# Kernel optimization log

Measured on AMD Instinct MI355X. Metric: run time of the kernel, lower is better.

## Reference

```python
import jax, jax.numpy as jnp
import numpy as np

N_NODES = 16384
K_NBR = 16
N_HOPS = 4  # hops + 2
IN_DIM = 256
RAW_DIM = 128
OUT_DIM = 64
PHI_DIM = 16
N_KERN = 4
E = N_NODES * K_NBR


def setup_inputs() -> dict:
    key = jax.random.key(0)
    ks = jax.random.split(key, 16)
    s = 0.05  # small weight scale for numerical sanity
    h = jax.random.normal(ks[0], (N_NODES, IN_DIM), jnp.float32)
    e_tensor = jax.random.normal(ks[1], (N_HOPS, N_NODES, RAW_DIM), jnp.float32)
    # kNN-style edges: each dst node has exactly K_NBR incoming edges
    src = jax.random.randint(ks[2], (N_HOPS, E), 0, N_NODES, jnp.int32)
    dst = jnp.tile(jnp.repeat(jnp.arange(N_NODES, dtype=jnp.int32), K_NBR)[None, :], (N_HOPS, 1))
    return {
        'h': h,
        'e_tensor': e_tensor,
        'src': src,
        'dst': dst,
        'W_phi': jax.random.normal(ks[3], (N_HOPS, RAW_DIM, PHI_DIM - 1), jnp.float32) * s,
        'mlp_w1': jax.random.normal(ks[4], (N_HOPS, RAW_DIM, IN_DIM), jnp.float32) * s,
        'mlp_b1': jax.random.normal(ks[5], (N_HOPS, IN_DIM), jnp.float32) * s,
        'mlp_w2': jax.random.normal(ks[6], (N_HOPS, IN_DIM, PHI_DIM * N_KERN), jnp.float32) * s,
        'mlp_b2': jax.random.normal(ks[7], (N_HOPS, PHI_DIM * N_KERN), jnp.float32) * s,
        'tilde_phi': jax.random.normal(ks[8], (N_HOPS, N_KERN, PHI_DIM), jnp.float32),
        'W': jax.random.normal(ks[9], (N_HOPS, IN_DIM, OUT_DIM * N_KERN), jnp.float32) * s,
        'bias': jax.random.normal(ks[10], (N_HOPS, OUT_DIM), jnp.float32) * s,
        'z': jax.random.normal(ks[11], (OUT_DIM, 1), jnp.float32),
    }


def _deform_gconv(h, e_l, src, dst, W_phi, w1, b1, w2, b2, tilde_phi, W, bias):
    N = h.shape[0]
    nk, phi_dim = tilde_phi.shape
    hk = (h @ W).reshape(N, nk, -1)                                  # (N, nk, out)
    phi = e_l @ W_phi                                                # (N, phi-1)
    tn = tilde_phi / jnp.linalg.norm(tilde_phi, axis=1, keepdims=True)  # (nk, phi)
    hid = jax.nn.relu(e_l @ w1 + b1)
    delta = (hid @ w2 + b2).reshape(N, nk, phi_dim)                  # (N, nk, phi)
    delta_ik = tn[None, :, :] + delta                                # (N, nk, phi)
    # per-edge quantities (edges carry dst-node delta_ik, u_sub_v distance)
    dist = phi[src] - phi[dst]                                       # (E, phi-1)
    last = jnp.all(dist == 0, axis=1, keepdims=True).astype(dist.dtype)
    dist = jnp.concatenate([dist, last], axis=1)                     # (E, phi)
    dist = dist / jnp.maximum(jnp.linalg.norm(dist, axis=1, keepdims=True), 1e-8)
    logits = jnp.einsum('ep,ekp->ek', dist, delta_ik[dst])           # (E, nk)
    # edge_softmax over incoming edges of each dst node
    mx = jax.ops.segment_max(logits, dst, num_segments=N)
    ex = jnp.exp(logits - mx[dst])
    den = jax.ops.segment_sum(ex, dst, num_segments=N)
    att = ex / den[dst]                                              # (E, nk)
    # message passing: m = h[src] * att, sum over incoming edges
    m = hk[src] * att[:, :, None]                                    # (E, nk, out)
    agg = jax.ops.segment_sum(m, dst, num_segments=N)                # (N, nk, out)
    out = agg.sum(1) + bias[None, :]
    out = out / jnp.maximum(jnp.linalg.norm(out, axis=1, keepdims=True), 1e-8)
    # regularizers
    d = tn[:, None, :] - tn[None, :, :]                              # (nk, nk, phi)
    l_sep = jnp.sum(jnp.sum(d * d, axis=-1)) / nk                    # sum_i mean_j ||t_i - t_j||^2
    l_focus = jnp.mean(jnp.sum(delta * delta, axis=2))
    return out, l_sep, l_focus


def reference(h, e_tensor, src, dst, W_phi, mlp_w1, mlp_b1, mlp_w2, mlp_b2, tilde_phi, W, bias, z):
    outs, l_seps, l_fos = jax.vmap(
        _deform_gconv, in_axes=(None, 0, 0, 0, 0, 0, 0, 0, 0, 0, 0, 0)
    )(h, e_tensor, src, dst, W_phi, mlp_w1, mlp_b1, mlp_w2, mlp_b2, tilde_phi, W, bias)
    # hop-level softmax fusion
    score = jnp.einsum('hno,oz->hnz', outs, z)                       # (n_hops, N, 1)
    att = jax.nn.softmax(score, axis=0)
    tilde_h = jnp.sum(att * outs, axis=0)                            # (N, out)
    l_sep = jnp.mean(l_seps)
    l_focus = jnp.mean(l_fos)
    return tilde_h, l_sep, l_focus
```

## Files before the change

kernel.cpp:

```cpp
#include <hip/hip_runtime.h>
#include <hip/hip_bf16.h>

#define N_NODES 16384
#define K_NBR 16
#define HOPS 4
#define IN_DIM 256
#define RAW_DIM 128
#define OUT_DIM 64
#define PHI_DIM 16
#define N_KERN 4
#define E_EDGES (N_NODES * K_NBR)

typedef __hip_bfloat16 bf16;
typedef __attribute__((ext_vector_type(8))) short short8;
typedef __attribute__((ext_vector_type(4))) float f32x4;
typedef __attribute__((ext_vector_type(4))) unsigned int uint4v;

__device__ __forceinline__ float toF(float x) { return x; }
__device__ __forceinline__ float toF(bf16 x) { return __bfloat162float(x); }
__device__ __forceinline__ short f2bfbits(float f)
{
    bf16 b = __float2bfloat16(f);
    short s; __builtin_memcpy(&s, &b, 2); return s;
}

#define SWZ(row, colShort) ((colShort) ^ (((row) & 7) << 3))

__device__ __forceinline__ void gld_lds16(const bf16* g, short* l)
{
    __builtin_amdgcn_global_load_lds(
        (const __attribute__((address_space(1))) unsigned int*)g,
        (__attribute__((address_space(3))) unsigned int*)l, 16, 0, 0);
}

#define CV_WPHI 0
#define CV_W1   (CV_WPHI + HOPS * RAW_DIM * (PHI_DIM - 1))
#define CV_B1   (CV_W1 + HOPS * RAW_DIM * IN_DIM)
#define CV_W2   (CV_B1 + HOPS * IN_DIM)
#define CV_B2   (CV_W2 + HOPS * IN_DIM * PHI_DIM * N_KERN)
#define CV_TPHI (CV_B2 + HOPS * PHI_DIM * N_KERN)
#define CV_W    (CV_TPHI + HOPS * N_KERN * PHI_DIM)
#define CV_BIAS (CV_W + HOPS * IN_DIM * OUT_DIM * N_KERN)
#define CV_Z    (CV_BIAS + HOPS * OUT_DIM)
#define CV_END  (CV_Z + OUT_DIM)

#define WT_N  (HOPS * 256 * 256)
#define W1T_N (HOPS * 256 * 128)
#define W2T_N (HOPS * 64 * 256)
#define WPT_N (HOPS * 16 * 128)
#define CVT_TOTAL (WT_N + W1T_N + W2T_N + WPT_N)

#define NB_CV ((CV_END + 255) / 256)
#define NB_WT (CVT_TOTAL / 256)
#define NB_H  (N_NODES * 256 / 8 / 256)
#define NB_E  (HOPS * N_NODES * 128 / 8 / 256)
#define NB_ALL (NB_CV + NB_WT + NB_H + NB_E + 1)

#define GA_NA 1536
#define GA_NB 1024
#define GA_TOTAL (GA_NA + GA_NB)

__device__ __forceinline__ float loadDyn(const void* p, int i, bool isbf)
{
    return isbf ? toF(((const bf16*)p)[i]) : ((const float*)p)[i];
}

__device__ __forceinline__ void cvt8(bf16* dst, const void* src, size_t base, bool isbf)
{
    short8 v;
    if (isbf) {
        v = *(const short8*)((const bf16*)src + base);
    } else {
        const float* sp = (const float*)src + base;
        f32x4 f0 = *(const f32x4*)sp;
        f32x4 f1 = *(const f32x4*)(sp + 4);
#pragma unroll
        for (int j = 0; j < 4; j++) { v[j] = f2bfbits(f0[j]); v[4 + j] = f2bfbits(f1[j]); }
    }
    *(short8*)(dst + base) = v;
}

__global__ __launch_bounds__(256) void cvt_all(
    const void* h, const void* e,
    const void* wphi, const void* w1, const void* b1, const void* w2,
    const void* b2, const void* tphi, const void* W, const void* bias,
    const void* z, float* __restrict__ CV,
    bf16* __restrict__ wt, bf16* __restrict__ w1t, bf16* __restrict__ w2t,
    bf16* __restrict__ wpt, bf16* __restrict__ h_bf, bf16* __restrict__ e_bf,
    float* __restrict__ tn_out, float* __restrict__ acc, int* __restrict__ flagOut)
{
    __shared__ float s_det[4];
    int tid = threadIdx.x;
    {
        unsigned short pv = ((const unsigned short*)h)[tid];
        unsigned int bits = ((unsigned int)pv) << 16;
        float v; __builtin_memcpy(&v, &bits, 4);
        v = fabsf(v);
        if (!(v == v) || v > 1e30f) v = 1e30f;
#pragma unroll
        for (int off = 32; off > 0; off >>= 1) v = fmaxf(v, __shfl_xor(v, off));
        if ((tid & 63) == 0) s_det[tid >> 6] = v;
    }
    __syncthreads();
    bool isbf = fmaxf(fmaxf(s_det[0], s_det[1]), fmaxf(s_det[2], s_det[3])) < 1e4f;

    int b = blockIdx.x;
    if (b == NB_ALL - 1) {
        __shared__ float s_v[256], s_tn[256], s_red[256], s_hop[4];
        int hop = tid >> 6, t64 = tid & 63;
        int row = t64 >> 4, p = t64 & 15;
        float v = loadDyn(tphi, hop * 64 + t64, isbf);
        s_v[tid] = v;
        __syncthreads();
        float ss = 0.f;
        for (int q = 0; q < 16; q++) { float x = s_v[hop * 64 + row * 16 + q]; ss += x * x; }
        float tnv = v / sqrtf(ss);
        tn_out[hop * 64 + t64] = tnv;
        s_tn[tid] = tnv;
        __syncthreads();
        float s = 0.f;
        for (int j = 0; j < 4; j++) {
            float d = tnv - s_tn[hop * 64 + j * 16 + p];
            s += d * d;
        }
        s_red[tid] = s;
        __syncthreads();
        if (t64 == 0) {
            float tot = 0.f;
            for (int i = 0; i < 64; i++) tot += s_red[hop * 64 + i];
            s_hop[hop] = tot;
        }
        __syncthreads();
        if (tid == 0) {
            acc[0] = (s_hop[0] + s_hop[1] + s_hop[2] + s_hop[3]) * 0.0625f;
            acc[1] = 0.f;
            *flagOut = isbf ? 1 : 0;
        }
        return;
    }
    if (b < NB_CV) {
        int idx = b * 256 + tid;
        if (idx >= CV_END) return;
        float v;
        if      (idx < CV_W1)   v = loadDyn(wphi, idx - CV_WPHI, isbf);
        else if (idx < CV_B1)   v = loadDyn(w1,   idx - CV_W1,   isbf);
        else if (idx < CV_W2)   v = loadDyn(b1,   idx - CV_B1,   isbf);
        else if (idx < CV_B2)   v = loadDyn(w2,   idx - CV_W2,   isbf);
        else if (idx < CV_TPHI) v = loadDyn(b2,   idx - CV_B2,   isbf);
        else if (idx < CV_W)    v = loadDyn(tphi, idx - CV_TPHI, isbf);
        else if (idx < CV_BIAS) v = loadDyn(W,    idx - CV_W,    isbf);
        else if (idx < CV_Z)    v = loadDyn(bias, idx - CV_BIAS, isbf);
        else                    v = loadDyn(z,    idx - CV_Z,    isbf);
        CV[idx] = v;
        return;
    }
    b -= NB_CV;
    if (b < NB_WT) {
        int idx = b * 256 + tid;
        if (idx < WT_N) {
            int o = idx, hop = o >> 16, rem = o & 65535, n = rem >> 8, k = rem & 255;
            wt[o] = __float2bfloat16(loadDyn(W, hop * 65536 + k * 256 + n, isbf));
        } else if (idx < WT_N + W1T_N) {
            int o = idx - WT_N, hop = o >> 15, rem = o & 32767, n = rem >> 7, k = rem & 127;
            w1t[o] = __float2bfloat16(loadDyn(w1, hop * 32768 + k * 256 + n, isbf));
        } else if (idx < WT_N + W1T_N + W2T_N) {
            int o = idx - WT_N - W1T_N, hop = o >> 14, rem = o & 16383, n = rem >> 8, k = rem & 255;
            w2t[o] = __float2bfloat16(loadDyn(w2, hop * 16384 + k * 64 + n, isbf));
        } else {
            int o = idx - WT_N - W1T_N - W2T_N, hop = o >> 11, rem = o & 2047, n = rem >> 7, k = rem & 127;
            float v = (n < 15) ? loadDyn(wphi, hop * 1920 + k * 15 + n, isbf) : 0.f;
            wpt[o] = __float2bfloat16(v);
        }
        return;
    }
    b -= NB_WT;
    if (b < NB_H) {
        size_t base = ((size_t)b * 256 + tid) * 8;
        cvt8(h_bf, h, base, isbf);
        return;
    }
    b -= NB_H;
    {
        size_t base = ((size_t)b * 256 + tid) * 8;
        cvt8(e_bf, e, base, isbf);
    }
}

template <int BN, int WR, int WC, int OUTMODE, bool STAGED>
__device__ __forceinline__ void gemm_dev(
    char* smem, const bf16* __restrict__ A, const bf16* __restrict__ Bt,
    void* __restrict__ Cg, int K, int N, int colBase, int rowBase)
{
    constexpr int WM = 128 / WR;
    constexpr int WN = BN / WC;
    constexpr int MT = WM / 16;
    constexpr int NT = WN / 16;
    constexpr int ESZ = (OUTMODE == 0) ? 4 : 1;
    short* As = (short*)smem;
    short* Bs = As + 128 * 64;

    int tid = threadIdx.x;
    int w = tid >> 6, lane = tid & 63;
    int wr = w / WC, wc = w % WC;
    int l16 = lane & 15, quad = lane >> 4;

    f32x4 acc[MT][NT] = {};

    for (int k0 = 0; k0 < K; k0 += 64) {
        for (int id = tid; id < 128 * 8; id += 256) {
            int row = id >> 3, j = id & 7;
            gld_lds16(A + (size_t)(rowBase + row) * K + k0 + ((j ^ (row & 7)) * 8),
                      As + id * 8);
        }
        for (int id = tid; id < BN * 8; id += 256) {
            int row = id >> 3, j = id & 7;
            gld_lds16(Bt + (size_t)(colBase + row) * K + k0 + ((j ^ (row & 7)) * 8),
                      Bs + id * 8);
        }
        __syncthreads();
#pragma unroll
        for (int kc = 0; kc < 64; kc += 32) {
            short8 aF[MT], bF[NT];
#pragma unroll
            for (int mi = 0; mi < MT; mi++) {
                int row = wr * WM + mi * 16 + l16;
                aF[mi] = *(const short8*)&As[row * 64 + SWZ(row, kc + quad * 8)];
            }
#pragma unroll
            for (int ni = 0; ni < NT; ni++) {
                int row = wc * WN + ni * 16 + l16;
                bF[ni] = *(const short8*)&Bs[row * 64 + SWZ(row, kc + quad * 8)];
            }
#pragma unroll
            for (int mi = 0; mi < MT; mi++)
#pragma unroll
                for (int ni = 0; ni < NT; ni++)
                    acc[mi][ni] = __builtin_amdgcn_mfma_f32_16x16x32_bf16(
                        aF[mi], bF[ni], acc[mi][ni], 0, 0, 0);
        }
        __syncthreads();
    }

#pragma unroll
    for (int mi = 0; mi < MT; mi++) {
#pragma unroll
        for (int ni = 0; ni < NT; ni++) {
            int cl = wc * WN + ni * 16 + l16;
            int col = colBase + cl;
#pragma unroll
            for (int r = 0; r < 4; r++) {
                int rl = wr * WM + mi * 16 + quad * 4 + r;
                float v = acc[mi][ni][r];
                if (STAGED) {
                    size_t idx = (size_t)rl * BN + cl;
                    if (OUTMODE == 0) ((float*)smem)[idx] = v;
                    else {
                        int pk = __builtin_amdgcn_cvt_pk_fp8_f32(v, v, 0, false);
                        ((unsigned char*)smem)[idx] = (unsigned char)(pk & 0xFF);
                    }
                } else {
                    ((float*)Cg)[(size_t)(rowBase + rl) * N + col] = v;
                }
            }
        }
    }
    if (STAGED) {
        __syncthreads();
        constexpr int CPR = BN * ESZ / 16;
        for (int c = tid; c < 128 * CPR; c += 256) {
            int r = c / CPR, off = (c % CPR) * 16;
            *(uint4v*)((char*)Cg + ((size_t)(rowBase + r) * N + colBase) * ESZ + off) =
                *(const uint4v*)(smem + (size_t)r * BN * ESZ + off);
        }
    }
}

__device__ __forceinline__ void hid_delta_dev(
    char* smem,
    const bf16* __restrict__ A, const bf16* __restrict__ B1,
    const bf16* __restrict__ B2, const float* __restrict__ b1,
    const float* __restrict__ b2, const float* __restrict__ tn,
    float* __restrict__ Dg, float* __restrict__ lfocus, int rowBase)
{
    short* As  = (short*)smem;
    short* Bs  = As + 64 * 64;
    short* Hs  = (short*)smem;
    short* B2s = Hs + 64 * 256;
    float* Ds  = (float*)smem;
    float* s_w = (float*)(smem + 64 * 256 * 2 + 64 * 64 * 2 - 16);

    int tid = threadIdx.x;
    int w = tid >> 6, lane = tid & 63;
    int l16 = lane & 15, quad = lane >> 4;

    {
        f32x4 acc[4][4] = {};
        for (int k0 = 0; k0 < 128; k0 += 64) {
            for (int id = tid; id < 64 * 8; id += 256) {
                int row = id >> 3, j = id & 7;
                gld_lds16(A + (size_t)(rowBase + row) * 128 + k0 + ((j ^ (row & 7)) * 8),
                          As + id * 8);
            }
            for (int id = tid; id < 256 * 8; id += 256) {
                int row = id >> 3, j = id & 7;
                gld_lds16(B1 + (size_t)row * 128 + k0 + ((j ^ (row & 7)) * 8),
                          Bs + id * 8);
            }
            __syncthreads();
#pragma unroll
            for (int kc = 0; kc < 64; kc += 32) {
                short8 aF[4], bF[4];
#pragma unroll
                for (int mi = 0; mi < 4; mi++) {
                    int row = mi * 16 + l16;
                    aF[mi] = *(const short8*)&As[row * 64 + SWZ(row, kc + quad * 8)];
                }
#pragma unroll
                for (int ni = 0; ni < 4; ni++) {
                    int row = w * 64 + ni * 16 + l16;
                    bF[ni] = *(const short8*)&Bs[row * 64 + SWZ(row, kc + quad * 8)];
                }
#pragma unroll
                for (int mi = 0; mi < 4; mi++)
#pragma unroll
                    for (int ni = 0; ni < 4; ni++)
                        acc[mi][ni] = __builtin_amdgcn_mfma_f32_16x16x32_bf16(
                            aF[mi], bF[ni], acc[mi][ni], 0, 0, 0);
            }
            __syncthreads();
        }
#pragma unroll
        for (int mi = 0; mi < 4; mi++) {
#pragma unroll
            for (int ni = 0; ni < 4; ni++) {
                int col = w * 64 + ni * 16 + l16;
                float bv = b1[col];
#pragma unroll
                for (int r = 0; r < 4; r++) {
                    int row = mi * 16 + quad * 4 + r;
                    float v = fmaxf(acc[mi][ni][r] + bv, 0.f);
                    Hs[row * 256 + SWZ(row, col)] = f2bfbits(v);
                }
            }
        }
        for (int id = tid; id < 64 * 8; id += 256) {
            int row = id >> 3, j = id & 7;
            gld_lds16(B2 + (size_t)row * 256 + ((j ^ (row & 7)) * 8),
                      B2s + id * 8);
        }
    }

    {
        f32x4 acc2[4] = {};
        for (int q = 0; q < 4; q++) {
            __syncthreads();
#pragma unroll
            for (int kcq = 0; kcq < 64; kcq += 32) {
                int arow = w * 16 + l16;
                short8 aF = *(const short8*)&Hs[arow * 256 + SWZ(arow, q * 64 + kcq + quad * 8)];
                short8 bF[4];
#pragma unroll
                for (int ni = 0; ni < 4; ni++) {
                    int row = ni * 16 + l16;
                    bF[ni] = *(const short8*)&B2s[row * 64 + SWZ(row, kcq + quad * 8)];
                }
#pragma unroll
                for (int ni = 0; ni < 4; ni++)
                    acc2[ni] = __builtin_amdgcn_mfma_f32_16x16x32_bf16(aF, bF[ni], acc2[ni], 0, 0, 0);
            }
            if (q < 3) {
                __syncthreads();
                for (int id = tid; id < 64 * 8; id += 256) {
                    int row = id >> 3, j = id & 7;
                    gld_lds16(B2 + (size_t)row * 256 + (q + 1) * 64 + ((j ^ (row & 7)) * 8),
                              B2s + id * 8);
                }
            }
        }
        __syncthreads();
        float sq = 0.f;
#pragma unroll
        for (int ni = 0; ni < 4; ni++) {
            int col = ni * 16 + l16;
            float bv = b2[col], tv = tn[col];
#pragma unroll
            for (int r = 0; r < 4; r++) {
                int row = w * 16 + quad * 4 + r;
                float v = acc2[ni][r] + bv;
                sq += v * v;
                Ds[row * 64 + col] = v + tv;
            }
        }
#pragma unroll
        for (int off = 32; off > 0; off >>= 1) sq += __shfl_xor(sq, off);
        if (lane == 0) s_w[w] = sq;
        __syncthreads();
        for (int c = tid; c < 64 * 16; c += 256) {
            int r = c >> 4, off = (c & 15) * 4;
            *(uint4v*)(Dg + (size_t)(rowBase + r) * 64 + off) =
                *(const uint4v*)(Ds + (size_t)r * 64 + off);
        }
        if (tid == 0) atomicAdd(lfocus, s_w[0] + s_w[1] + s_w[2] + s_w[3]);
    }
}

__global__ __launch_bounds__(256) void gemm_all(
    const bf16* __restrict__ h_bf, const bf16* __restrict__ e_bf,
    const bf16* __restrict__ WT, const bf16* __restrict__ WPT,
    const bf16* __restrict__ W1T, const bf16* __restrict__ W2T,
    const float* __restrict__ b1All, const float* __restrict__ b2All,
    const float* __restrict__ tnAll, unsigned char* __restrict__ hk_f8,
    float* __restrict__ phi, float* __restrict__ DELTA, float* __restrict__ lfocus)
{
    __shared__ __align__(16) char smem[64 * 256 * 2 + 64 * 64 * 2];
    int b = blockIdx.x;
    bool isA;
    int a;
    if (b < 2 * GA_NB) { isA = !(b & 1); a = b >> 1; }
    else               { isA = true;     a = GA_NB + (b - 2 * GA_NB); }
    if (isA) {
        int hop = a / 384, r = a % 384, part = r >> 7, row = r & 127;
        if (part < 2) {
            gemm_dev<128, 2, 2, 2, true>(
                smem, h_bf, WT + (size_t)hop * 256 * 256,
                hk_f8 + (size_t)hop * N_NODES * 256, 256, 256, part * 128, row * 128);
        } else {
            gemm_dev<16, 4, 1, 0, false>(
                smem, e_bf + (size_t)hop * N_NODES * 128, WPT + (size_t)hop * 16 * 128,
                phi + (size_t)hop * N_NODES * 16, 128, 16, 0, row * 128);
        }
    } else {
        int hop = a >> 8, tile = a & 255;
        hid_delta_dev(smem,
            e_bf + (size_t)hop * N_NODES * 128,
            W1T + (size_t)hop * 256 * 128, W2T + (size_t)hop * 64 * 256,
            b1All + hop * 256, b2All + hop * 64, tnAll + hop * 64,
            DELTA + (size_t)hop * N_NODES * 64, lfocus, tile * 64);
    }
}

__global__ __launch_bounds__(256) void edge_agg2(
    const unsigned char* __restrict__ hk, const float* __restrict__ phi,
    const float* __restrict__ dik, const int* __restrict__ src,
    const float* __restrict__ biasAll, float* __restrict__ outs)
{
    int b = blockIdx.x;
    int hop = b & 3;
    int wave = threadIdx.x >> 6, lane = threadIdx.x & 63;
    int node = (b >> 2) * 4 + wave;
    const unsigned char* hk_l = hk + (size_t)hop * N_NODES * 256;
    const float* phi_l  = phi + (size_t)hop * N_NODES * 16;
    const float* dik_l  = dik + (size_t)hop * N_NODES * 64;
    const int*   src_n  = src + (size_t)hop * E_EDGES + (size_t)node * 16;
    const float* bias_l = biasAll + hop * 64;
    float*       outs_n = outs + ((size_t)hop * N_NODES + node) * 64;

    __shared__ float s_dik[4][64];
    __shared__ __align__(16) float s_attT[4][4][24];
    __shared__ int   s_src[4][16];

    s_dik[wave][lane] = dik_l[(size_t)node * 64 + lane];
    if (lane < 16) s_src[wave][lane] = src_n[lane];

    int e = lane >> 2, q = lane & 3;
    int sN = s_src[wave][e];
    f32x4 ps = *(const f32x4*)(phi_l + (size_t)sN * 16 + q * 4);
    f32x4 pd = *(const f32x4*)(phi_l + (size_t)node * 16 + q * 4);
    float d0 = ps[0] - pd[0], d1 = ps[1] - pd[1];
    float d2 = ps[2] - pd[2], d3 = ps[3] - pd[3];
    bool q3 = (q == 3);
    float ssp = d0 * d0 + d1 * d1 + d2 * d2 + (q3 ? 0.f : d3 * d3);
    ssp += __shfl_xor(ssp, 1); ssp += __shfl_xor(ssp, 2);
    float last = (ssp == 0.f) ? 1.f : 0.f;
    if (q3) d3 = last;
    float inv = 1.f / fmaxf(sqrtf(ssp + last * last), 1e-8f);
#pragma unroll
    for (int k = 0; k < 4; k++) {
        const float* dk = &s_dik[wave][k * 16 + q * 4];
        float pk = d0 * dk[0] + d1 * dk[1] + d2 * dk[2] + d3 * dk[3];
        pk += __shfl_xor(pk, 1); pk += __shfl_xor(pk, 2);
        if (q == k) s_attT[wave][k][e] = pk * inv;
    }

    int k2 = lane & 3;
    float lgv = s_attT[wave][k2][e];
    float mx = lgv;
    mx = fmaxf(mx, __shfl_xor(mx, 4));
    mx = fmaxf(mx, __shfl_xor(mx, 8));
    mx = fmaxf(mx, __shfl_xor(mx, 16));
    mx = fmaxf(mx, __shfl_xor(mx, 32));
    float ex = __expf(lgv - mx);
    float den = ex;
    den += __shfl_xor(den, 4);
    den += __shfl_xor(den, 8);
    den += __shfl_xor(den, 16);
    den += __shfl_xor(den, 32);
    s_attT[wave][k2][e] = ex / den;

    int kk = lane >> 4, dsub = (lane & 15) * 4;
    f32x4 attv[4];
#pragma unroll
    for (int g = 0; g < 4; g++) attv[g] = *(const f32x4*)&s_attT[wave][kk][g * 4];
    float a0 = 0.f, a1 = 0.f, a2 = 0.f, a3 = 0.f;
#pragma unroll
    for (int ee = 0; ee < 16; ee++) {
        int sm = __builtin_amdgcn_readfirstlane(s_src[wave][ee]);
        unsigned int u = *(const unsigned int*)(hk_l + (size_t)sm * 256 + lane * 4);
        float wgt = attv[ee >> 2][ee & 3];
        auto lo = __builtin_amdgcn_cvt_pk_f32_fp8((int)u, false);
        auto hi = __builtin_amdgcn_cvt_pk_f32_fp8((int)u, true);
        a0 += wgt * lo[0];
        a1 += wgt * lo[1];
        a2 += wgt * hi[0];
        a3 += wgt * hi[1];
    }
    a0 += __shfl_xor(a0, 16); a0 += __shfl_xor(a0, 32);
    a1 += __shfl_xor(a1, 16); a1 += __shfl_xor(a1, 32);
    a2 += __shfl_xor(a2, 16); a2 += __shfl_xor(a2, 32);
    a3 += __shfl_xor(a3, 16); a3 += __shfl_xor(a3, 32);
    f32x4 bv = *(const f32x4*)(bias_l + dsub);
    float o0 = a0 + bv[0];
    float o1 = a1 + bv[1];
    float o2 = a2 + bv[2];
    float o3 = a3 + bv[3];
    float ssq = o0 * o0 + o1 * o1 + o2 * o2 + o3 * o3;
    ssq += __shfl_xor(ssq, 1);
    ssq += __shfl_xor(ssq, 2);
    ssq += __shfl_xor(ssq, 4);
    ssq += __shfl_xor(ssq, 8);
    float inv2 = 1.f / fmaxf(sqrtf(ssq), 1e-8f);
    if (kk == 0) {
        f32x4 st;
        st[0] = o0 * inv2; st[1] = o1 * inv2; st[2] = o2 * inv2; st[3] = o3 * inv2;
        *(f32x4*)(outs_n + dsub) = st;
    }
}

__global__ __launch_bounds__(256) void fuse_kernel(
    const float* __restrict__ outs, const float* __restrict__ z,
    void* __restrict__ out, const int* __restrict__ flag,
    const float* __restrict__ acc)
{
    int tid = threadIdx.x;
    int node = blockIdx.x * 4 + (tid >> 6);
    int dd = tid & 63;
    float zv = z[dd];
    float o[4], sc[4];
#pragma unroll
    for (int h = 0; h < 4; h++) {
        o[h] = outs[((size_t)h * N_NODES + node) * 64 + dd];
        float v = o[h] * zv;
#pragma unroll
        for (int off = 32; off > 0; off >>= 1) v += __shfl_xor(v, off);
        sc[h] = v;
    }
    float mx = fmaxf(fmaxf(sc[0], sc[1]), fmaxf(sc[2], sc[3]));
    float e0 = __expf(sc[0] - mx), e1 = __expf(sc[1] - mx);
    float e2 = __expf(sc[2] - mx), e3 = __expf(sc[3] - mx);
    float den = e0 + e1 + e2 + e3;
    float t = (e0 * o[0] + e1 * o[1] + e2 * o[2] + e3 * o[3]) / den;
    size_t oi = (size_t)node * 64 + dd;
    bool isbf = (*flag != 0);
    if (isbf) ((bf16*)out)[oi] = __float2bfloat16(t);
    else      ((float*)out)[oi] = t;
    if (blockIdx.x == 0 && tid == 0) {
        float a = acc[0];
        float b = acc[1] / ((float)N_NODES * 4.f * 4.f);
        size_t base = (size_t)N_NODES * 64;
        if (isbf) {
            ((bf16*)out)[base]     = __float2bfloat16(a);
            ((bf16*)out)[base + 1] = __float2bfloat16(b);
        } else {
            ((float*)out)[base]     = a;
            ((float*)out)[base + 1] = b;
        }
    }
}

extern "C" void kernel_launch(void* const* d_in, const int* in_sizes, int n_in,
                              void* d_out, int out_size, void* d_ws, size_t ws_size,
                              hipStream_t stream)
{
    const void* h    = d_in[0];
    const void* e    = d_in[1];
    const int*  src  = (const int*)d_in[2];
    const void* Wphi = d_in[4];
    const void* w1   = d_in[5];
    const void* b1   = d_in[6];
    const void* w2   = d_in[7];
    const void* b2   = d_in[8];
    const void* tphi = d_in[9];
    const void* W    = d_in[10];
    const void* bias = d_in[11];
    const void* z    = d_in[12];

    float* ws    = (float*)d_ws;
    float* CV    = ws;
    float* OUTS  = CV + CV_END;
    float* PHI   = OUTS + (size_t)4 * N_NODES * 64;
    float* DELTA = PHI + (size_t)4 * N_NODES * 16;
    float* TN    = DELTA + (size_t)4 * N_NODES * 64;
    float* ACC   = TN + 256;
    int*   FLAG  = (int*)(ACC + 2);
    bf16*  H_BF  = (bf16*)(ACC + 4);
    bf16*  E_BF  = H_BF + (size_t)N_NODES * 256;
    bf16*  WT    = E_BF + (size_t)HOPS * N_NODES * 128;
    bf16*  W1T   = WT + WT_N;
    bf16*  W2T   = W1T + W1T_N;
    bf16*  WPT   = W2T + W2T_N;
    unsigned char* HK_F8 = (unsigned char*)(WPT + WPT_N);

    cvt_all<<<NB_ALL, 256, 0, stream>>>(
        h, e, Wphi, w1, b1, w2, b2, tphi, W, bias, z, CV,
        WT, W1T, W2T, WPT, H_BF, E_BF, TN, ACC, FLAG);

    gemm_all<<<dim3(GA_TOTAL), 256, 0, stream>>>(
        H_BF, E_BF, WT, WPT, W1T, W2T,
        CV + CV_B1, CV + CV_B2, TN, HK_F8, PHI, DELTA, ACC + 1);

    edge_agg2<<<dim3(N_NODES), 256, 0, stream>>>(
        HK_F8, PHI, DELTA, src, CV + CV_BIAS, OUTS);

    fuse_kernel<<<dim3(N_NODES / 4), 256, 0, stream>>>(
        OUTS, CV + CV_Z, d_out, FLAG, ACC);
}
```

Before: 208.6 us.

## Fuse phi projection into hidden-delta GEMM and double-buffer hk GEMM

The separate phi GEMM blocks are removed. Wave 0 of the hid/delta blocks now computes phi = e @ W_phi with extra MFMAs while the same e tile sits in shared memory, which cuts redundant loads of e and the block count. The hk GEMM is specialised to K=256 and double-buffers its shared-memory A/B tiles so the next tile's loads overlap the MFMAs on the current one. Shared memory per block grows to 64KB, which may lower occupancy, and only wave 0 does the phi work, adding imbalance across waves.

New measurement: 200.7 us. -3.8%, faster.

```diff
diff --git a/kernel.cpp b/kernel.cpp
--- a/kernel.cpp
+++ b/kernel.cpp
@@ -56,9 +56,7 @@
 #define NB_E  (HOPS * N_NODES * 128 / 8 / 256)
 #define NB_ALL (NB_CV + NB_WT + NB_H + NB_E + 1)
 
-#define GA_NA 1536
-#define GA_NB 1024
-#define GA_TOTAL (GA_NA + GA_NB)
+#define GA_TOTAL 2048
 
 __device__ __forceinline__ float loadDyn(const void* p, int i, bool isbf)
 {
@@ -186,108 +184,100 @@
     }
 }
 
-template <int BN, int WR, int WC, int OUTMODE, bool STAGED>
-__device__ __forceinline__ void gemm_dev(
+__device__ __forceinline__ void gemm_hk_dev(
     char* smem, const bf16* __restrict__ A, const bf16* __restrict__ Bt,
-    void* __restrict__ Cg, int K, int N, int colBase, int rowBase)
-{
-    constexpr int WM = 128 / WR;
-    constexpr int WN = BN / WC;
-    constexpr int MT = WM / 16;
-    constexpr int NT = WN / 16;
-    constexpr int ESZ = (OUTMODE == 0) ? 4 : 1;
-    short* As = (short*)smem;
-    short* Bs = As + 128 * 64;
-
+    unsigned char* __restrict__ Cg, int colBase, int rowBase)
+{
+    short* base = (short*)smem;
     int tid = threadIdx.x;
     int w = tid >> 6, lane = tid & 63;
-    int wr = w / WC, wc = w % WC;
+    int wr = w >> 1, wc = w & 1;
     int l16 = lane & 15, quad = lane >> 4;
-
-    f32x4 acc[MT][NT] = {};
-
-    for (int k0 = 0; k0 < K; k0 += 64) {
-        for (int id = tid; id < 128 * 8; id += 256) {
-            int row = id >> 3, j = id & 7;
-            gld_lds16(A + (size_t)(rowBase + row) * K + k0 + ((j ^ (row & 7)) * 8),
-                      As + id * 8);
-        }
-        for (int id = tid; id < BN * 8; id += 256) {
-            int row = id >> 3, j = id & 7;
-            gld_lds16(Bt + (size_t)(colBase + row) * K + k0 + ((j ^ (row & 7)) * 8),
-                      Bs + id * 8);
-        }
-        __syncthreads();
+    f32x4 acc[4][4] = {};
+
+#define HK_STAGE(bufb, k0v)                                                          \
+    {                                                                                \
+        short* As_ = base + (bufb) * 16384;                                          \
+        short* Bs_ = As_ + 8192;                                                     \
+        for (int id = tid; id < 128 * 8; id += 256) {                                \
+            int row = id >> 3, j = id & 7;                                           \
+            gld_lds16(A + (size_t)(rowBase + row) * 256 + (k0v) + ((j ^ (row & 7)) * 8), \
+                      As_ + id * 8);                                                 \
+        }                                                                            \
+        for (int id = tid; id < 128 * 8; id += 256) {                                \
+            int row = id >> 3, j = id & 7;                                           \
+            gld_lds16(Bt + (size_t)(colBase + row) * 256 + (k0v) + ((j ^ (row & 7)) * 8), \
+                      Bs_ + id * 8);                                                 \
+        }                                                                            \
+    }
+
+    HK_STAGE(0, 0)
+    __syncthreads();
+    for (int t = 0; t < 4; ++t) {
+        if (t < 3) HK_STAGE((t + 1) & 1, (t + 1) * 64)
+        short* As = base + (t & 1) * 16384;
+        short* Bs = As + 8192;
 #pragma unroll
         for (int kc = 0; kc < 64; kc += 32) {
-            short8 aF[MT], bF[NT];
-#pragma unroll
-            for (int mi = 0; mi < MT; mi++) {
-                int row = wr * WM + mi * 16 + l16;
+            short8 aF[4], bF[4];
+#pragma unroll
+            for (int mi = 0; mi < 4; mi++) {
+                int row = wr * 64 + mi * 16 + l16;
                 aF[mi] = *(const short8*)&As[row * 64 + SWZ(row, kc + quad * 8)];
             }
 #pragma unroll
-            for (int ni = 0; ni < NT; ni++) {
-                int row = wc * WN + ni * 16 + l16;
+            for (int ni = 0; ni < 4; ni++) {
+                int row = wc * 64 + ni * 16 + l16;
                 bF[ni] = *(const short8*)&Bs[row * 64 + SWZ(row, kc + quad * 8)];
             }
 #pragma unroll
-            for (int mi = 0; mi < MT; mi++)
-#pragma unroll
-                for (int ni = 0; ni < NT; ni++)
+            for (int mi = 0; mi < 4; mi++)
+#pragma unroll
+                for (int ni = 0; ni < 4; ni++)
                     acc[mi][ni] = __builtin_amdgcn_mfma_f32_16x16x32_bf16(
                         aF[mi], bF[ni], acc[mi][ni], 0, 0, 0);
         }
         __syncthreads();
     }
-
-#pragma unroll
-    for (int mi = 0; mi < MT; mi++) {
-#pragma unroll
-        for (int ni = 0; ni < NT; ni++) {
-            int cl = wc * WN + ni * 16 + l16;
-            int col = colBase + cl;
+#undef HK_STAGE
+
+    unsigned char* Cs = (unsigned char*)smem;
+#pragma unroll
+    for (int mi = 0; mi < 4; mi++)
+#pragma unroll
+        for (int ni = 0; ni < 4; ni++) {
+            int cl = wc * 64 + ni * 16 + l16;
 #pragma unroll
             for (int r = 0; r < 4; r++) {
-                int rl = wr * WM + mi * 16 + quad * 4 + r;
+                int rl = wr * 64 + mi * 16 + quad * 4 + r;
                 float v = acc[mi][ni][r];
-                if (STAGED) {
-                    size_t idx = (size_t)rl * BN + cl;
-                    if (OUTMODE == 0) ((float*)smem)[idx] = v;
-                    else {
-                        int pk = __builtin_amdgcn_cvt_pk_fp8_f32(v, v, 0, false);
-                        ((unsigned char*)smem)[idx] = (unsigned char)(pk & 0xFF);
-                    }
-                } else {
-                    ((float*)Cg)[(size_t)(rowBase + rl) * N + col] = v;
-                }
-            }
-        }
-    }
-    if (STAGED) {
-        __syncthreads();
-        constexpr int CPR = BN * ESZ / 16;
-        for (int c = tid; c < 128 * CPR; c += 256) {
-            int r = c / CPR, off = (c % CPR) * 16;
-            *(uint4v*)((char*)Cg + ((size_t)(rowBase + r) * N + colBase) * ESZ + off) =
-                *(const uint4v*)(smem + (size_t)r * BN * ESZ + off);
-        }
+                int pk = __builtin_amdgcn_cvt_pk_fp8_f32(v, v, 0, false);
+                Cs[rl * 128 + cl] = (unsigned char)(pk & 0xFF);
+            }
+        }
+    __syncthreads();
+    for (int c = tid; c < 128 * 8; c += 256) {
+        int r = c >> 3, off = (c & 7) * 16;
+        *(uint4v*)(Cg + ((size_t)(rowBase + r) * 256 + colBase) + off) =
+            *(const uint4v*)(Cs + (size_t)r * 128 + off);
     }
 }
 
 __device__ __forceinline__ void hid_delta_dev(
     char* smem,
     const bf16* __restrict__ A, const bf16* __restrict__ B1,
-    const bf16* __restrict__ B2, const float* __restrict__ b1,
-    const float* __restrict__ b2, const float* __restrict__ tn,
-    float* __restrict__ Dg, float* __restrict__ lfocus, int rowBase)
+    const bf16* __restrict__ B2, const bf16* __restrict__ WP,
+    const float* __restrict__ b1, const float* __restrict__ b2,
+    const float* __restrict__ tn, float* __restrict__ Dg,
+    float* __restrict__ phiG, float* __restrict__ lfocus, int rowBase)
 {
     short* As  = (short*)smem;
     short* Bs  = As + 64 * 64;
+    short* Wpa = As + 20480;
     short* Hs  = (short*)smem;
     short* B2s = Hs + 64 * 256;
     float* Ds  = (float*)smem;
-    float* s_w = (float*)(smem + 64 * 256 * 2 + 64 * 64 * 2 - 16);
+    float* s_w = (float*)(smem + 40944);
 
     int tid = threadIdx.x;
     int w = tid >> 6, lane = tid & 63;
@@ -295,6 +285,7 @@
 
     {
         f32x4 acc[4][4] = {};
+        f32x4 accp[4] = {};
         for (int k0 = 0; k0 < 128; k0 += 64) {
             for (int id = tid; id < 64 * 8; id += 256) {
                 int row = id >> 3, j = id & 7;
@@ -306,6 +297,11 @@
                 gld_lds16(B1 + (size_t)row * 128 + k0 + ((j ^ (row & 7)) * 8),
                           Bs + id * 8);
             }
+            if (k0 == 0) {
+                int row = tid >> 4, j = tid & 15;
+                gld_lds16(WP + (size_t)row * 128 + ((j ^ (row & 7)) * 8),
+                          Wpa + tid * 8);
+            }
             __syncthreads();
 #pragma unroll
             for (int kc = 0; kc < 64; kc += 32) {
@@ -326,6 +322,13 @@
                     for (int ni = 0; ni < 4; ni++)
                         acc[mi][ni] = __builtin_amdgcn_mfma_f32_16x16x32_bf16(
                             aF[mi], bF[ni], acc[mi][ni], 0, 0, 0);
+                if (w == 0) {
+                    short8 bFp = *(const short8*)&Wpa[l16 * 128 + SWZ(l16, k0 + kc + quad * 8)];
+#pragma unroll
+                    for (int mi = 0; mi < 4; mi++)
+                        accp[mi] = __builtin_amdgcn_mfma_f32_16x16x32_bf16(
+                            aF[mi], bFp, accp[mi], 0, 0, 0);
+                }
             }
             __syncthreads();
         }
@@ -347,6 +350,14 @@
             int row = id >> 3, j = id & 7;
             gld_lds16(B2 + (size_t)row * 256 + ((j ^ (row & 7)) * 8),
                       B2s + id * 8);
+        }
+        if (w == 0) {
+#pragma unroll
+            for (int mi = 0; mi < 4; mi++)
+#pragma unroll
+                for (int r = 0; r < 4; r++)
+                    phiG[(size_t)(rowBase + mi * 16 + quad * 4 + r) * 16 + l16] =
+                        accp[mi][r];
         }
     }
 
@@ -412,30 +423,23 @@
     const float* __restrict__ tnAll, unsigned char* __restrict__ hk_f8,
     float* __restrict__ phi, float* __restrict__ DELTA, float* __restrict__ lfocus)
 {
-    __shared__ __align__(16) char smem[64 * 256 * 2 + 64 * 64 * 2];
+    __shared__ __align__(16) char smem[65536];
     int b = blockIdx.x;
-    bool isA;
-    int a;
-    if (b < 2 * GA_NB) { isA = !(b & 1); a = b >> 1; }
-    else               { isA = true;     a = GA_NB + (b - 2 * GA_NB); }
-    if (isA) {
-        int hop = a / 384, r = a % 384, part = r >> 7, row = r & 127;
-        if (part < 2) {
-            gemm_dev<128, 2, 2, 2, true>(
-                smem, h_bf, WT + (size_t)hop * 256 * 256,
-                hk_f8 + (size_t)hop * N_NODES * 256, 256, 256, part * 128, row * 128);
-        } else {
-            gemm_dev<16, 4, 1, 0, false>(
-                smem, e_bf + (size_t)hop * N_NODES * 128, WPT + (size_t)hop * 16 * 128,
-                phi + (size_t)hop * N_NODES * 16, 128, 16, 0, row * 128);
-        }
+    int a = b >> 1;
+    int hop = a >> 8;
+    if (!(b & 1)) {
+        int r = a & 255, part = r >> 7, row = r & 127;
+        gemm_hk_dev(smem, h_bf, WT + (size_t)hop * 65536,
+                    hk_f8 + (size_t)hop * N_NODES * 256, part * 128, row * 128);
     } else {
-        int hop = a >> 8, tile = a & 255;
+        int tile = a & 255;
         hid_delta_dev(smem,
             e_bf + (size_t)hop * N_NODES * 128,
-            W1T + (size_t)hop * 256 * 128, W2T + (size_t)hop * 64 * 256,
+            W1T + (size_t)hop * 32768, W2T + (size_t)hop * 16384,
+            WPT + (size_t)hop * 2048,
             b1All + hop * 256, b2All + hop * 64, tnAll + hop * 64,
-            DELTA + (size_t)hop * N_NODES * 64, lfocus, tile * 64);
+            DELTA + (size_t)hop * N_NODES * 64,
+            phi + (size_t)hop * N_NODES * 16, lfocus, tile * 64);
     }
 }
 
```
